# Kernel optimization log

Hardware: AMD Instinct MI355X
Metric: run time of the kernel (lower is better)

The kernel has to match this reference:

```python
import jax, jax.numpy as jnp
import numpy as np

N, E = 25000, 400000
F, D, H, C, L = 64, 128, 4, 128, 3  # in_feat, hidden, heads, per-head dim, layers
SCALE = 1.0 / np.sqrt(C)

_PNAMES = [f"{nm}{l}" for l in range(L) for nm in ("Wq", "bq", "Wk", "bk", "Wv", "bv", "Ws", "bs")]


def setup_inputs() -> dict:
    key = jax.random.key(0)
    ks = jax.random.split(key, 64)
    inp = {
        "x": jax.random.normal(ks[0], (N, F), jnp.float32),
        "edge_index": jax.random.randint(ks[1], (2, E), 0, N, jnp.int32),
    }
    i = 2
    for l in range(L):
        fin = F if l == 0 else D
        s = 1.0 / np.sqrt(fin)
        shapes = {"Wq": (fin, H * C), "bq": (H * C,), "Wk": (fin, H * C), "bk": (H * C,),
                  "Wv": (fin, H * C), "bv": (H * C,), "Ws": (fin, D), "bs": (D,)}
        for nm, shp in shapes.items():
            scale = s if nm.startswith("W") else 0.01
            inp[f"{nm}{l}"] = jax.random.normal(ks[i], shp, jnp.float32) * scale
            i += 1
    inp["Wfc"] = jax.random.normal(ks[i], (D, 1), jnp.float32) * (1.0 / np.sqrt(D))
    inp["bfc"] = jnp.zeros((1,), jnp.float32)
    return inp


def _conv(x, src, dst, Wq, bq, Wk, bk, Wv, bv, Ws, bs):
    """PyG TransformerConv, heads=H, concat=False (head-mean), root_weight=True."""
    n = x.shape[0]
    q = (x @ Wq + bq).reshape(n, H, C)
    k = (x @ Wk + bk).reshape(n, H, C)
    v = (x @ Wv + bv).reshape(n, H, C)
    # per-edge attention logits: query at dst, key at src  -> [E, H]
    alpha = jnp.einsum("ehc,ehc->eh", q[dst], k[src]) * SCALE
    # scatter-softmax over incoming edges of each destination node
    m = jax.ops.segment_max(alpha, dst, num_segments=n)        # [N, H]
    e = jnp.exp(alpha - m[dst])                                 # [E, H]
    denom = jax.ops.segment_sum(e, dst, num_segments=n)        # [N, H]
    a = e / (denom[dst] + 1e-16)                                # [E, H]
    out = jax.ops.segment_sum(a[:, :, None] * v[src], dst, num_segments=n)  # [N, H, C]
    return out.mean(axis=1) + x @ Ws + bs                       # concat=False -> mean heads; + skip


def reference(x, edge_index,
              Wq0, bq0, Wk0, bk0, Wv0, bv0, Ws0, bs0,
              Wq1, bq1, Wk1, bk1, Wv1, bv1, Ws1, bs1,
              Wq2, bq2, Wk2, bk2, Wv2, bv2, Ws2, bs2,
              Wfc, bfc):
    src, dst = edge_index[0], edge_index[1]
    h = jax.nn.relu(_conv(x, src, dst, Wq0, bq0, Wk0, bk0, Wv0, bv0, Ws0, bs0))
    h = jax.nn.relu(_conv(h, src, dst, Wq1, bq1, Wk1, bk1, Wv1, bv1, Ws1, bs1))
    h = jax.nn.relu(_conv(h, src, dst, Wq2, bq2, Wk2, bk2, Wv2, bv2, Ws2, bs2))
    g = h.mean(axis=0, keepdims=True)                           # [1, D]
    return jax.nn.sigmoid(g @ Wfc + bfc)                        # [1, 1]
```

## Files before the change

kernel.cpp:

```cpp
#include <hip/hip_runtime.h>
#include <hip/hip_bf16.h>
#include <math.h>

#define NNODES 25000
#define NEDGES 400000
#define FIN0 64
#define DHID 128
#define NHEAD 4
#define CDIM 128
#define HC (NHEAD * CDIM)
#define NOUT 1664
#define SCALE 0.088388347648318447f

typedef __attribute__((ext_vector_type(8))) short short8;
typedef __attribute__((ext_vector_type(4))) float floatx4;
typedef __attribute__((ext_vector_type(2))) float fx2;

__device__ __forceinline__ short f2bf(float v) {
    unsigned u = __float_as_uint(v);
    u = (u + 0x7fffu + ((u >> 16) & 1u)) >> 16;
    return (short)u;
}
__device__ __forceinline__ float bf2f(short s) {
    return __uint_as_float(((unsigned)(unsigned short)s) << 16);
}


__global__ void zero_int_kernel(int* __restrict__ p, int n) {
    int i = blockIdx.x * blockDim.x + threadIdx.x;
    if (i < n) p[i] = 0;
}

__global__ void zero_float_kernel(float* __restrict__ p, int n) {
    int i = blockIdx.x * blockDim.x + threadIdx.x;
    if (i < n) p[i] = 0.f;
}

__global__ void cvt_x_kernel(const float* __restrict__ x, short* __restrict__ xb, int total) {
    int i = blockIdx.x * blockDim.x + threadIdx.x;
    if (i < total) xb[i] = f2bf(x[i]);
}

__global__ void cvt_w_kernel(const float* __restrict__ Wq, const float* __restrict__ Wk,
                             const float* __restrict__ Wv, const float* __restrict__ Ws,
                             const float* __restrict__ bq, const float* __restrict__ bk,
                             const float* __restrict__ bv, const float* __restrict__ bs,
                             short* __restrict__ WT, float* __restrict__ bc, int finShift) {
    int idx = blockIdx.x * blockDim.x + threadIdx.x;
    int fin = 1 << finShift;
    int total = NOUT << finShift;
    if (idx < total) {
        int c = idx >> finShift;
        int k = idx & (fin - 1);
        float v;
        if (c < 512)       v = Wq[k * 512 + c];
        else if (c < 1024) v = Wk[k * 512 + c - 512];
        else if (c < 1536) v = Wv[k * 512 + c - 1024];
        else               v = Ws[k * 128 + c - 1536];
        WT[idx] = f2bf(v);
    }
    if (idx < NOUT) {
        int c = idx;
        float b;
        if (c < 512)       b = bq[c];
        else if (c < 1024) b = bk[c - 512];
        else if (c < 1536) b = bv[c - 1024];
        else               b = bs[c - 1536];
        bc[c] = b;
    }
}


__global__ void count_kernel(const int* __restrict__ dst, int* __restrict__ deg, int e) {
    int i = blockIdx.x * blockDim.x + threadIdx.x;
    if (i < e) atomicAdd(&deg[dst[i]], 1);
}

__global__ void scan_kernel(const int* __restrict__ deg, int* __restrict__ offs,
                            int* __restrict__ cnt, int n, int total) {
    __shared__ int sums[256];
    int t = threadIdx.x;
    int chunk = (n + 255) / 256;
    int b = t * chunk;
    int e = min(b + chunk, n);
    int s = 0;
    for (int i = b; i < e; ++i) s += deg[i];
    sums[t] = s;
    __syncthreads();
    for (int o = 1; o < 256; o <<= 1) {
        int v = (t >= o) ? sums[t - o] : 0;
        __syncthreads();
        sums[t] += v;
        __syncthreads();
    }
    int run = sums[t] - s;
    for (int i = b; i < e; ++i) {
        offs[i] = run;
        run += deg[i];
        cnt[i] = 0;
    }
    if (t == 0) offs[n] = total;
}

__global__ void scatter_kernel(const int* __restrict__ src, const int* __restrict__ dst,
                               const int* __restrict__ offs, int* __restrict__ cnt,
                               int* __restrict__ csr, int e) {
    int i = blockIdx.x * blockDim.x + threadIdx.x;
    if (i < e) {
        int d = dst[i];
        int pos = offs[d] + atomicAdd(&cnt[d], 1);
        csr[pos] = src[i];
    }
}

__global__ __launch_bounds__(256) void gemm_qkvs_mfma(
    const short* __restrict__ Xb, int n, int finShift,
    const short* __restrict__ WT, const float* __restrict__ bc,
    short* __restrict__ Qb, unsigned char* __restrict__ KV,
    float* __restrict__ S)
{
    __shared__ short Xs[64][136];
    __shared__ short Wt[64][136];

    int t = threadIdx.x;
    int row0 = blockIdx.x * 64, col0 = blockIdx.y * 64;
    int fin = 1 << finShift;
    int cs = finShift - 3;
    int cmask = (1 << cs) - 1;

    for (int i = t; i < (64 << cs); i += 256) {
        int r = i >> cs, c = (i & cmask) * 8;
        int gr = row0 + r;
        uint4 v = make_uint4(0u, 0u, 0u, 0u);
        if (gr < n) v = *(const uint4*)&Xb[(size_t)gr * fin + c];
        *(uint4*)&Xs[r][c] = v;
    }
    for (int i = t; i < (64 << cs); i += 256) {
        int r = i >> cs, c = (i & cmask) * 8;
        *(uint4*)&Wt[r][c] = *(const uint4*)&WT[((size_t)(col0 + r) << finShift) + c];
    }
    __syncthreads();

    int l = t & 63, w = t >> 6;
    int wr = (w >> 1) * 32, wc = (w & 1) * 32;
    int lr = l & 15, lk = (l >> 4) * 8;

    floatx4 acc[2][2] = {};
    for (int k0 = 0; k0 < fin; k0 += 32) {
        short8 a0 = *(const short8*)&Xs[wr + lr][k0 + lk];
        short8 a1 = *(const short8*)&Xs[wr + 16 + lr][k0 + lk];
        short8 b0 = *(const short8*)&Wt[wc + lr][k0 + lk];
        short8 b1 = *(const short8*)&Wt[wc + 16 + lr][k0 + lk];
        acc[0][0] = __builtin_amdgcn_mfma_f32_16x16x32_bf16(a0, b0, acc[0][0], 0, 0, 0);
        acc[0][1] = __builtin_amdgcn_mfma_f32_16x16x32_bf16(a0, b1, acc[0][1], 0, 0, 0);
        acc[1][0] = __builtin_amdgcn_mfma_f32_16x16x32_bf16(a1, b0, acc[1][0], 0, 0, 0);
        acc[1][1] = __builtin_amdgcn_mfma_f32_16x16x32_bf16(a1, b1, acc[1][1], 0, 0, 0);
    }

    int rb = (l >> 4) * 4;
    int cl = l & 15;
#pragma unroll
    for (int mi = 0; mi < 2; ++mi) {
#pragma unroll
        for (int ni = 0; ni < 2; ++ni) {
            int gc = col0 + wc + ni * 16 + cl;
            float bias = bc[gc];
#pragma unroll
            for (int r = 0; r < 4; ++r) {
                int gr = row0 + wr + mi * 16 + rb + r;
                if (gr < n) {
                    float v = acc[mi][ni][r] + bias;
                    if (gc < 512) {
                        Qb[(size_t)gr * 512 + gc] = f2bf(v);
                    } else if (gc < 1536) {
                        int idx = (gc < 1024) ? (gc - 512) : (512 + gc - 1024);
                        unsigned enc = (unsigned)__builtin_amdgcn_cvt_pk_fp8_f32(v, v, 0, false);
                        KV[(size_t)gr * 1024 + idx] = (unsigned char)enc;
                    } else {
                        S[(size_t)gr * 128 + gc - 1536] = v;
                    }
                }
            }
        }
    }
}


__device__ __forceinline__ void unpack8(uint4 r, float* f) {
    f[0] = __uint_as_float(r.x << 16);
    f[1] = __uint_as_float(r.x & 0xffff0000u);
    f[2] = __uint_as_float(r.y << 16);
    f[3] = __uint_as_float(r.y & 0xffff0000u);
    f[4] = __uint_as_float(r.z << 16);
    f[5] = __uint_as_float(r.z & 0xffff0000u);
    f[6] = __uint_as_float(r.w << 16);
    f[7] = __uint_as_float(r.w & 0xffff0000u);
}

__device__ __forceinline__ void decf8(uint2 r, float* f) {
    fx2 a = __builtin_amdgcn_cvt_pk_f32_fp8(r.x, false);
    fx2 b = __builtin_amdgcn_cvt_pk_f32_fp8(r.x, true);
    fx2 c = __builtin_amdgcn_cvt_pk_f32_fp8(r.y, false);
    fx2 d = __builtin_amdgcn_cvt_pk_f32_fp8(r.y, true);
    f[0] = a[0]; f[1] = a[1]; f[2] = b[0]; f[3] = b[1];
    f[4] = c[0]; f[5] = c[1]; f[6] = d[0]; f[7] = d[1];
}

__device__ __forceinline__ float dotf8(const float* q, uint2 r) {
    float f[8];
    decf8(r, f);
    float p = 0.f;
#pragma unroll
    for (int j = 0; j < 8; ++j) p = fmaf(q[j], f[j], p);
    return p;
}

__device__ __forceinline__ void updf8(float& m, float& d, float* acc,
                                      float alpha, uint2 vr) {
    float vf[8];
    decf8(vr, vf);
    float nm = fmaxf(m, alpha);
    float sc = __expf(m - nm);
    float w  = __expf(alpha - nm);
    d = d * sc + w;
#pragma unroll
    for (int j = 0; j < 8; ++j) acc[j] = acc[j] * sc + w * vf[j];
    m = nm;
}

__global__ __launch_bounds__(256) void attn_kernel(
    const short* __restrict__ Qb, const unsigned char* __restrict__ KV,
    const int* __restrict__ offs, const int* __restrict__ csr,
    const float* __restrict__ S, short* __restrict__ Xo, int n)
{
    int node = (blockIdx.x * blockDim.x + threadIdx.x) >> 6;
    if (node >= n) return;
    int lane = threadIdx.x & 63;

    float qf[8];
    {
        uint4 qr = *(const uint4*)&Qb[(size_t)node * 512 + lane * 8];
        unpack8(qr, qf);
    }

    int beg = offs[node], end = offs[node + 1];
    float m = -INFINITY, d = 0.f;
    float acc[8] = {};

    int e = beg;
    for (; e + 3 < end; e += 4) {
        int s0 = csr[e], s1 = csr[e + 1], s2 = csr[e + 2], s3 = csr[e + 3];
        const unsigned char* b0 = KV + (size_t)s0 * 1024 + lane * 8;
        const unsigned char* b1 = KV + (size_t)s1 * 1024 + lane * 8;
        const unsigned char* b2 = KV + (size_t)s2 * 1024 + lane * 8;
        const unsigned char* b3 = KV + (size_t)s3 * 1024 + lane * 8;
        uint2 k0 = *(const uint2*)b0;
        uint2 k1 = *(const uint2*)b1;
        uint2 k2 = *(const uint2*)b2;
        uint2 k3 = *(const uint2*)b3;
        uint2 v0 = *(const uint2*)(b0 + 512);
        uint2 v1 = *(const uint2*)(b1 + 512);
        uint2 v2 = *(const uint2*)(b2 + 512);
        uint2 v3 = *(const uint2*)(b3 + 512);
        float p0 = dotf8(qf, k0);
        float p1 = dotf8(qf, k1);
        float p2 = dotf8(qf, k2);
        float p3 = dotf8(qf, k3);
#pragma unroll
        for (int o = 1; o < 16; o <<= 1) {
            p0 += __shfl_xor(p0, o);
            p1 += __shfl_xor(p1, o);
            p2 += __shfl_xor(p2, o);
            p3 += __shfl_xor(p3, o);
        }
        updf8(m, d, acc, p0 * SCALE, v0);
        updf8(m, d, acc, p1 * SCALE, v1);
        updf8(m, d, acc, p2 * SCALE, v2);
        updf8(m, d, acc, p3 * SCALE, v3);
    }
    for (; e < end; ++e) {
        int s0 = csr[e];
        const unsigned char* b0 = KV + (size_t)s0 * 1024 + lane * 8;
        uint2 k0 = *(const uint2*)b0;
        uint2 v0 = *(const uint2*)(b0 + 512);
        float p0 = dotf8(qf, k0);
#pragma unroll
        for (int o = 1; o < 16; o <<= 1) p0 += __shfl_xor(p0, o);
        updf8(m, d, acc, p0 * SCALE, v0);
    }

    float inv = (d > 0.f) ? 1.f / d : 0.f;
#pragma unroll
    for (int j = 0; j < 8; ++j) acc[j] *= inv;

#pragma unroll
    for (int j = 0; j < 8; ++j) {
        acc[j] += __shfl_xor(acc[j], 16);
        acc[j] += __shfl_xor(acc[j], 32);
    }

    if (lane < 16) {
        int c0 = lane * 8;
        const float* Srow = S + (size_t)node * 128 + c0;
        short8 o;
#pragma unroll
        for (int j = 0; j < 8; ++j)
            o[j] = f2bf(fmaxf(acc[j] * 0.25f + Srow[j], 0.f));
        *(short8*)&Xo[(size_t)node * 128 + c0] = o;
    }
}

__global__ void colsum_kernel(const short* __restrict__ X, float* __restrict__ g, int n) {
    int c = threadIdx.x;
    int rpb = (n + gridDim.x - 1) / gridDim.x;
    int r0 = blockIdx.x * rpb;
    int r1 = min(r0 + rpb, n);
    float acc = 0.f;
    for (int r = r0; r < r1; ++r) acc += bf2f(X[r * DHID + c]);
    atomicAdd(&g[c], acc);
}

__global__ void final_kernel(const float* __restrict__ g, const float* __restrict__ Wfc,
                             const float* __restrict__ bfc, float* __restrict__ out, float invn) {
    __shared__ float red[128];
    int t = threadIdx.x;
    red[t] = g[t] * invn * Wfc[t];
    __syncthreads();
    for (int o = 64; o > 0; o >>= 1) {
        if (t < o) red[t] += red[t + o];
        __syncthreads();
    }
    if (t == 0) {
        float z = red[0] + bfc[0];
        out[0] = 1.f / (1.f + expf(-z));
    }
}


extern "C" void kernel_launch(void* const* d_in, const int* in_sizes, int n_in,
                              void* d_out, int out_size, void* d_ws, size_t ws_size,
                              hipStream_t stream) {
    const int N = NNODES, E = NEDGES;
    const float* x = (const float*)d_in[0];
    const int* ei = (const int*)d_in[1];
    const int* src = ei;
    const int* dst = ei + E;
    const float* Wfc = (const float*)d_in[26];
    const float* bfc = (const float*)d_in[27];

    size_t off = 0;
    auto alloc = [&](size_t bytes) -> char* {
        char* p = (char*)d_ws + off;
        off += (bytes + 255) & ~(size_t)255;
        return p;
    };
    int* deg   = (int*)alloc((size_t)N * 4);
    int* cnt   = (int*)alloc((size_t)N * 4);
    int* offs  = (int*)alloc((size_t)(N + 1) * 4);
    int* csr   = (int*)alloc((size_t)E * 4);
    short* Qb  = (short*)alloc((size_t)N * HC * 2);
    unsigned char* KV = (unsigned char*)alloc((size_t)N * 1024);
    float* S   = (float*)alloc((size_t)N * DHID * 4);
    short* xb0 = (short*)alloc((size_t)N * FIN0 * 2);
    short* xb1 = (short*)alloc((size_t)N * DHID * 2);
    short* xb2 = (short*)alloc((size_t)N * DHID * 2);
    short* WT  = (short*)alloc((size_t)NOUT * DHID * 2);
    float* bc  = (float*)alloc((size_t)NOUT * 4);
    float* g   = (float*)alloc(128 * 4);

    zero_int_kernel<<<(N + 255) / 256, 256, 0, stream>>>(deg, N);
    zero_float_kernel<<<1, 128, 0, stream>>>(g, 128);
    count_kernel<<<(E + 255) / 256, 256, 0, stream>>>(dst, deg, E);
    scan_kernel<<<1, 256, 0, stream>>>(deg, offs, cnt, N, E);
    scatter_kernel<<<(E + 255) / 256, 256, 0, stream>>>(src, dst, offs, cnt, csr, E);

    cvt_x_kernel<<<(N * FIN0 + 255) / 256, 256, 0, stream>>>(x, xb0, N * FIN0);

    int attn_blocks = (N + 3) / 4;

    const short* xin = xb0;
    short* xouts[3] = { xb1, xb2, xb1 };
    for (int l = 0; l < 3; ++l) {
        int finShift = (l == 0) ? 6 : 7;
        int fin = 1 << finShift;
        const float* Wq = (const float*)d_in[2 + l * 8 + 0];
        const float* bq = (const float*)d_in[2 + l * 8 + 1];
        const float* Wk = (const float*)d_in[2 + l * 8 + 2];
        const float* bk = (const float*)d_in[2 + l * 8 + 3];
        const float* Wv = (const float*)d_in[2 + l * 8 + 4];
        const float* bv = (const float*)d_in[2 + l * 8 + 5];
        const float* Wss= (const float*)d_in[2 + l * 8 + 6];
        const float* bs = (const float*)d_in[2 + l * 8 + 7];

        cvt_w_kernel<<<(NOUT * fin + 255) / 256, 256, 0, stream>>>(
            Wq, Wk, Wv, Wss, bq, bk, bv, bs, WT, bc, finShift);

        dim3 ggrid((N + 63) / 64, NOUT / 64);
        gemm_qkvs_mfma<<<ggrid, 256, 0, stream>>>(xin, N, finShift, WT, bc, Qb, KV, S);
        attn_kernel<<<attn_blocks, 256, 0, stream>>>(Qb, KV, offs, csr, S, xouts[l], N);
        xin = xouts[l];
    }

    colsum_kernel<<<256, 128, 0, stream>>>(xb1, g, N);
    final_kernel<<<1, 128, 0, stream>>>(g, Wfc, bfc, (float*)d_out, 1.0f / N);
}
```

Measured before the change: 620.4 us.

## Enlarge GEMM tile to 128x128, template on input width, store skip term as bf16

```diff
diff --git a/kernel.cpp b/kernel.cpp
--- a/kernel.cpp
+++ b/kernel.cpp
@@ -113,72 +113,82 @@
     }
 }
 
+template<int FIN>
 __global__ __launch_bounds__(256) void gemm_qkvs_mfma(
-    const short* __restrict__ Xb, int n, int finShift,
+    const short* __restrict__ Xb, int n,
     const short* __restrict__ WT, const float* __restrict__ bc,
     short* __restrict__ Qb, unsigned char* __restrict__ KV,
-    float* __restrict__ S)
+    short* __restrict__ Sb)
 {
-    __shared__ short Xs[64][136];
-    __shared__ short Wt[64][136];
+    constexpr int PITCH = FIN + 8;
+    constexpr int CSH = (FIN == 128) ? 4 : 3;
+    constexpr int CMASK = (1 << CSH) - 1;
+
+    __shared__ short Xs[128][PITCH];
+    __shared__ short Wt[128][PITCH];
 
     int t = threadIdx.x;
-    int row0 = blockIdx.x * 64, col0 = blockIdx.y * 64;
-    int fin = 1 << finShift;
-    int cs = finShift - 3;
-    int cmask = (1 << cs) - 1;
-
-    for (int i = t; i < (64 << cs); i += 256) {
-        int r = i >> cs, c = (i & cmask) * 8;
+    int row0 = blockIdx.x * 128;
+    int y = blockIdx.y;
+    int col0 = y * 128;
+
+    for (int i = t; i < (128 << CSH); i += 256) {
+        int r = i >> CSH, c = (i & CMASK) * 8;
         int gr = row0 + r;
         uint4 v = make_uint4(0u, 0u, 0u, 0u);
-        if (gr < n) v = *(const uint4*)&Xb[(size_t)gr * fin + c];
+        if (gr < n) v = *(const uint4*)&Xb[(size_t)gr * FIN + c];
         *(uint4*)&Xs[r][c] = v;
     }
-    for (int i = t; i < (64 << cs); i += 256) {
-        int r = i >> cs, c = (i & cmask) * 8;
-        *(uint4*)&Wt[r][c] = *(const uint4*)&WT[((size_t)(col0 + r) << finShift) + c];
+    for (int i = t; i < (128 << CSH); i += 256) {
+        int r = i >> CSH, c = (i & CMASK) * 8;
+        *(uint4*)&Wt[r][c] = *(const uint4*)&WT[(size_t)(col0 + r) * FIN + c];
     }
     __syncthreads();
 
     int l = t & 63, w = t >> 6;
-    int wr = (w >> 1) * 32, wc = (w & 1) * 32;
+    int wr = (w >> 1) * 64, wc = (w & 1) * 64;
     int lr = l & 15, lk = (l >> 4) * 8;
 
-    floatx4 acc[2][2] = {};
-    for (int k0 = 0; k0 < fin; k0 += 32) {
-        short8 a0 = *(const short8*)&Xs[wr + lr][k0 + lk];
-        short8 a1 = *(const short8*)&Xs[wr + 16 + lr][k0 + lk];
-        short8 b0 = *(const short8*)&Wt[wc + lr][k0 + lk];
-        short8 b1 = *(const short8*)&Wt[wc + 16 + lr][k0 + lk];
-        acc[0][0] = __builtin_amdgcn_mfma_f32_16x16x32_bf16(a0, b0, acc[0][0], 0, 0, 0);
-        acc[0][1] = __builtin_amdgcn_mfma_f32_16x16x32_bf16(a0, b1, acc[0][1], 0, 0, 0);
-        acc[1][0] = __builtin_amdgcn_mfma_f32_16x16x32_bf16(a1, b0, acc[1][0], 0, 0, 0);
-        acc[1][1] = __builtin_amdgcn_mfma_f32_16x16x32_bf16(a1, b1, acc[1][1], 0, 0, 0);
-    }
-
-    int rb = (l >> 4) * 4;
-    int cl = l & 15;
-#pragma unroll
-    for (int mi = 0; mi < 2; ++mi) {
-#pragma unroll
-        for (int ni = 0; ni < 2; ++ni) {
+    floatx4 acc[4][4] = {};
+    for (int k0 = 0; k0 < FIN; k0 += 32) {
+        short8 a[4], b[4];
+#pragma unroll
+        for (int mi = 0; mi < 4; ++mi)
+            a[mi] = *(const short8*)&Xs[wr + mi * 16 + lr][k0 + lk];
+#pragma unroll
+        for (int ni = 0; ni < 4; ++ni)
+            b[ni] = *(const short8*)&Wt[wc + ni * 16 + lr][k0 + lk];
+#pragma unroll
+        for (int mi = 0; mi < 4; ++mi)
+#pragma unroll
+            for (int ni = 0; ni < 4; ++ni)
+                acc[mi][ni] = __builtin_amdgcn_mfma_f32_16x16x32_bf16(
+                    a[mi], b[ni], acc[mi][ni], 0, 0, 0);
+    }
+
+    int rb = (l >> 4) * 4, cl = l & 15;
+    int kind = (y < 4) ? 0 : (y < 8) ? 1 : (y < 12) ? 2 : 3;
+#pragma unroll
+    for (int mi = 0; mi < 4; ++mi) {
+#pragma unroll
+        for (int ni = 0; ni < 4; ++ni) {
             int gc = col0 + wc + ni * 16 + cl;
             float bias = bc[gc];
 #pragma unroll
             for (int r = 0; r < 4; ++r) {
                 int gr = row0 + wr + mi * 16 + rb + r;
-                if (gr < n) {
-                    float v = acc[mi][ni][r] + bias;
-                    if (gc < 512) {
-                        Qb[(size_t)gr * 512 + gc] = f2bf(v);
-                    } else if (gc < 1536) {
-                        int idx = (gc < 1024) ? (gc - 512) : (512 + gc - 1024);
-                        unsigned enc = (unsigned)__builtin_amdgcn_cvt_pk_fp8_f32(v, v, 0, false);
-                        KV[(size_t)gr * 1024 + idx] = (unsigned char)enc;
-                    } else {
-                        S[(size_t)gr * 128 + gc - 1536] = v;
-                    }
+                if (gr >= n) continue;
+                float v = acc[mi][ni][r] + bias;
+                if (kind == 0) {
+                    Qb[(size_t)gr * 512 + gc] = f2bf(v);
+                } else if (kind == 1) {
+                    unsigned enc = (unsigned)__builtin_amdgcn_cvt_pk_fp8_f32(v, v, 0, false);
+                    KV[(size_t)gr * 1024 + (gc - 512)] = (unsigned char)enc;
+                } else if (kind == 2) {
+                    unsigned enc = (unsigned)__builtin_amdgcn_cvt_pk_fp8_f32(v, v, 0, false);
+                    KV[(size_t)gr * 1024 + 512 + (gc - 1024)] = (unsigned char)enc;
+                } else {
+                    Sb[(size_t)gr * 128 + (gc - 1536)] = f2bf(v);
                 }
             }
         }
@@ -231,7 +241,7 @@
 __global__ __launch_bounds__(256) void attn_kernel(
     const short* __restrict__ Qb, const unsigned char* __restrict__ KV,
     const int* __restrict__ offs, const int* __restrict__ csr,
-    const float* __restrict__ S, short* __restrict__ Xo, int n)
+    const short* __restrict__ Sb, short* __restrict__ Xo, int n)
 {
     int node = (blockIdx.x * blockDim.x + threadIdx.x) >> 6;
     if (node >= n) return;
@@ -301,11 +311,13 @@
 
     if (lane < 16) {
         int c0 = lane * 8;
-        const float* Srow = S + (size_t)node * 128 + c0;
+        float sf[8];
+        uint4 sr = *(const uint4*)&Sb[(size_t)node * 128 + c0];
+        unpack8(sr, sf);
         short8 o;
 #pragma unroll
         for (int j = 0; j < 8; ++j)
-            o[j] = f2bf(fmaxf(acc[j] * 0.25f + Srow[j], 0.f));
+            o[j] = f2bf(fmaxf(acc[j] * 0.25f + sf[j], 0.f));
         *(short8*)&Xo[(size_t)node * 128 + c0] = o;
     }
 }
@@ -360,7 +372,7 @@
     int* csr   = (int*)alloc((size_t)E * 4);
     short* Qb  = (short*)alloc((size_t)N * HC * 2);
     unsigned char* KV = (unsigned char*)alloc((size_t)N * 1024);
-    float* S   = (float*)alloc((size_t)N * DHID * 4);
+    short* Sb  = (short*)alloc((size_t)N * DHID * 2);
     short* xb0 = (short*)alloc((size_t)N * FIN0 * 2);
     short* xb1 = (short*)alloc((size_t)N * DHID * 2);
     short* xb2 = (short*)alloc((size_t)N * DHID * 2);
@@ -395,9 +407,12 @@
         cvt_w_kernel<<<(NOUT * fin + 255) / 256, 256, 0, stream>>>(
             Wq, Wk, Wv, Wss, bq, bk, bv, bs, WT, bc, finShift);
 
-        dim3 ggrid((N + 63) / 64, NOUT / 64);
-        gemm_qkvs_mfma<<<ggrid, 256, 0, stream>>>(xin, N, finShift, WT, bc, Qb, KV, S);
-        attn_kernel<<<attn_blocks, 256, 0, stream>>>(Qb, KV, offs, csr, S, xouts[l], N);
+        dim3 ggrid((N + 127) / 128, 13);
+        if (l == 0)
+            gemm_qkvs_mfma<64><<<ggrid, 256, 0, stream>>>(xin, N, WT, bc, Qb, KV, Sb);
+        else
+            gemm_qkvs_mfma<128><<<ggrid, 256, 0, stream>>>(xin, N, WT, bc, Qb, KV, Sb);
+        attn_kernel<<<attn_blocks, 256, 0, stream>>>(Qb, KV, offs, csr, Sb, xouts[l], N);
         xin = xouts[l];
     }
 
```

Measured after the change: 609.5 us. Within noise of the previous version (-1.8%).
